# Kernel optimization log

Measured on AMD Instinct MI355X. Metric: run time of the kernel, lower is better.

## Reference

```python
import jax, jax.numpy as jnp
import numpy as np

N = 10000      # nodes
E = 160000     # edges (before self loops)
F_IN = 78      # atom features
C = 128        # output_dim per head
H = 10         # heads in gat1
G = 64         # graphs in batch


def gat_conv(x, src, dst, n_nodes, W, a_src, a_dst, heads, ch):
    # x: [N, Fin]; W: [Fin, heads*ch]; a_src/a_dst: [heads, ch]
    h = (x @ W).reshape(-1, heads, ch)                      # [N, H, C]
    alpha_src = (h * a_src).sum(-1)                         # [N, H]
    alpha_dst = (h * a_dst).sum(-1)                         # [N, H]
    e = jax.nn.leaky_relu(alpha_src[src] + alpha_dst[dst], 0.2)  # [E, H]
    # segment softmax over edges grouped by destination node
    m = jax.ops.segment_max(e, dst, num_segments=n_nodes)
    m = jnp.where(jnp.isfinite(m), m, 0.0)
    ex = jnp.exp(e - m[dst])
    den = jax.ops.segment_sum(ex, dst, num_segments=n_nodes)
    alpha = ex / (den[dst] + 1e-16)                         # [E, H]
    out = jax.ops.segment_sum(h[src] * alpha[:, :, None], dst,
                              num_segments=n_nodes)          # [N, H, C]
    return out, alpha


def setup_inputs() -> dict:
    key = jax.random.key(0)
    ks = jax.random.split(key, 12)
    x = jax.random.normal(ks[0], (N, F_IN), dtype=jnp.float32)
    edge_index = jax.random.randint(ks[1], (2, E), 0, N, dtype=jnp.int64)
    batch = jnp.sort(jax.random.randint(ks[2], (N,), 0, G, dtype=jnp.int64))
    s1 = 1.0 / np.sqrt(F_IN)
    s2 = 1.0 / np.sqrt(H * C)
    W1 = jax.random.normal(ks[3], (F_IN, H * C), jnp.float32) * s1
    att_src1 = jax.random.normal(ks[4], (H, C), jnp.float32) * 0.1
    att_dst1 = jax.random.normal(ks[5], (H, C), jnp.float32) * 0.1
    b1 = jnp.zeros((H * C,), jnp.float32)
    W2 = jax.random.normal(ks[6], (H * C, C), jnp.float32) * s2
    att_src2 = jax.random.normal(ks[7], (1, C), jnp.float32) * 0.1
    att_dst2 = jax.random.normal(ks[8], (1, C), jnp.float32) * 0.1
    b2 = jnp.zeros((C,), jnp.float32)
    return {"x": x, "edge_index": edge_index, "batch": batch,
            "W1": W1, "att_src1": att_src1, "att_dst1": att_dst1, "b1": b1,
            "W2": W2, "att_src2": att_src2, "att_dst2": att_dst2, "b2": b2}


def reference(x, edge_index, batch, W1, att_src1, att_dst1, b1,
              W2, att_src2, att_dst2, b2):
    n = x.shape[0]
    loops = jnp.arange(n, dtype=edge_index.dtype)
    src = jnp.concatenate([edge_index[0], loops])  # PyG adds self loops
    dst = jnp.concatenate([edge_index[1], loops])
    # layer 1: 10 heads, concat
    h1, alpha1 = gat_conv(x, src, dst, n, W1, att_src1, att_dst1, H, C)
    h1 = jax.nn.elu(h1.reshape(n, H * C) + b1)     # dropout skipped (eval)
    # layer 2: 1 head
    h2, _ = gat_conv(h1, src, dst, n, W2, att_src2, att_dst2, 1, C)
    h2 = jax.nn.elu(h2.reshape(n, C) + b2)
    # global max pool per graph
    pooled = jax.ops.segment_max(h2, batch, num_segments=G)  # [G, C]
    return pooled, alpha1
```

## Files before the change

kernel.cpp:

```cpp
#include <hip/hip_runtime.h>
#include <hip/hip_bf16.h>

#define FIN 78
#define CDIM 128
#define HEADS 10
#define HC 1280
#define GRAPHS 64
#define KP 96

typedef __bf16 bf16x8 __attribute__((ext_vector_type(8)));
typedef __bf16 bf16x4 __attribute__((ext_vector_type(4)));
typedef float f32x4 __attribute__((ext_vector_type(4)));

__global__ void init_kernel(unsigned* counts, unsigned* cursor, unsigned* pooled_u,
                            float* as1, float* ad1,
                            const float* __restrict__ x, __bf16* __restrict__ xb,
                            const float* __restrict__ W1, __bf16* __restrict__ W1t,
                            const float* __restrict__ W2, __bf16* __restrict__ W2t,
                            int N, int Mpad) {
    int t = blockIdx.x * 256 + threadIdx.x;
    if (t < N) { counts[t] = 0u; cursor[t] = 0u; }
    if (t < GRAPHS * CDIM) pooled_u[t] = 0x007FFFFFu;
    if (t < N * HEADS) { as1[t] = 0.f; ad1[t] = 0.f; }
    if (t < Mpad * KP) {
        int m = t / KP, k = t % KP;
        float v = (m < N && k < FIN) ? x[(size_t)m * FIN + k] : 0.f;
        xb[t] = (__bf16)v;
    }
    if (t < HC * KP) {
        int n = t / KP, k = t % KP;
        float v = (k < FIN) ? W1[(size_t)k * HC + n] : 0.f;
        W1t[t] = (__bf16)v;
    }
    if (t < CDIM * HC) {
        int n = t / HC, k = t % HC;
        W2t[t] = (__bf16)W2[(size_t)k * CDIM + n];
    }
}

__global__ __launch_bounds__(256) void gemm1_mfma_kernel(
        const __bf16* __restrict__ xb, const __bf16* __restrict__ W1t,
        const float* __restrict__ asrc, const float* __restrict__ adst,
        __bf16* __restrict__ h1pb, float* __restrict__ as1, float* __restrict__ ad1,
        int M) {
    __shared__ __align__(16) __bf16 smem[2 * 128 * 104];
    auto Alds = (__bf16 (*)[104])smem;
    auto Blds = (__bf16 (*)[104])(smem + 128 * 104);
    const int tid = threadIdx.x;
    const int wave = tid >> 6, lane = tid & 63;
    const int wr = wave >> 1, wc = wave & 1;
    const int m0 = blockIdx.x * 128;
    const int head = blockIdx.y;
    const int n0 = head * CDIM;
    const int fl = lane & 15;
    const int fh = lane >> 4;

    for (int idx = tid; idx < 128 * 12; idx += 256) {
        int r = idx / 12, ks = (idx % 12) * 8;
        *(bf16x8*)&Alds[r][ks] = *(const bf16x8*)(xb + (size_t)(m0 + r) * KP + ks);
        *(bf16x8*)&Blds[r][ks] = *(const bf16x8*)(W1t + (size_t)(n0 + r) * KP + ks);
    }
    __syncthreads();

    f32x4 acc[4][4] = {};
    #pragma unroll
    for (int ks = 0; ks < KP; ks += 32) {
        bf16x8 a[4], b[4];
        #pragma unroll
        for (int t = 0; t < 4; ++t) {
            a[t] = *(const bf16x8*)&Alds[wr * 64 + t * 16 + fl][ks + fh * 8];
            b[t] = *(const bf16x8*)&Blds[wc * 64 + t * 16 + fl][ks + fh * 8];
        }
        #pragma unroll
        for (int i = 0; i < 4; ++i)
            #pragma unroll
            for (int j = 0; j < 4; ++j)
                acc[i][j] = __builtin_amdgcn_mfma_f32_16x16x32_bf16(a[i], b[j], acc[i][j], 0, 0, 0);
    }

    float a_s[4], a_d[4];
    #pragma unroll
    for (int j = 0; j < 4; ++j) {
        int gn = n0 + wc * 64 + j * 16 + fl;
        a_s[j] = asrc[gn];
        a_d[j] = adst[gn];
    }
    #pragma unroll
    for (int i = 0; i < 4; ++i) {
        #pragma unroll
        for (int r = 0; r < 4; ++r) {
            int gm = m0 + wr * 64 + i * 16 + fh * 4 + r;
            float vs = 0.f, vd = 0.f;
            #pragma unroll
            for (int j = 0; j < 4; ++j) {
                vs += acc[i][j][r] * a_s[j];
                vd += acc[i][j][r] * a_d[j];
            }
            #pragma unroll
            for (int off = 1; off < 16; off <<= 1) {
                vs += __shfl_xor(vs, off);
                vd += __shfl_xor(vd, off);
            }
            if (fl == 0 && gm < M) {
                atomicAdd(&as1[gm * HEADS + head], vs);
                atomicAdd(&ad1[gm * HEADS + head], vd);
            }
        }
    }

    __syncthreads();
    auto Cst = (__bf16 (*)[136])smem;
    #pragma unroll
    for (int i = 0; i < 4; ++i)
        #pragma unroll
        for (int j = 0; j < 4; ++j)
            #pragma unroll
            for (int r = 0; r < 4; ++r)
                Cst[wr * 64 + i * 16 + fh * 4 + r][wc * 64 + j * 16 + fl] = (__bf16)acc[i][j][r];
    __syncthreads();
    for (int idx = tid; idx < 128 * 16; idx += 256) {
        int r = idx >> 4, v = (idx & 15) * 8;
        int gm = m0 + r;
        if (gm < M)
            *(bf16x8*)(h1pb + (size_t)gm * HC + n0 + v) = *(const bf16x8*)&Cst[r][v];
    }
}

__global__ __launch_bounds__(256) void gemm2_mfma_kernel(
        const __bf16* __restrict__ A, const __bf16* __restrict__ W2t,
        float* __restrict__ Cpart, int M) {
    constexpr int BK = 64;
    constexpr int KCHUNK = HC / 2;
    __shared__ __align__(16) __bf16 smem[2 * 64 * 72];
    auto Alds = (__bf16 (*)[72])smem;
    auto Blds = (__bf16 (*)[72])(smem + 64 * 72);
    const int tid = threadIdx.x;
    const int wave = tid >> 6, lane = tid & 63;
    const int wr = wave >> 1, wc = wave & 1;
    const int m0 = blockIdx.x * 64;
    const int n0 = blockIdx.y * 64;
    const int kbase = blockIdx.z * KCHUNK;

    const int kslot = (tid & 7) * 8;
    const int srow  = tid >> 3;
    const int fl = lane & 15;
    const int fh = lane >> 4;

    f32x4 acc[2][2] = {};

    for (int k0 = kbase; k0 < kbase + KCHUNK; k0 += BK) {
        #pragma unroll
        for (int rp = 0; rp < 2; ++rp) {
            int r = srow + rp * 32;
            int gm = m0 + r;
            bf16x8 va = {};
            if (gm < M) va = *(const bf16x8*)(A + (size_t)gm * HC + k0 + kslot);
            *(bf16x8*)&Alds[r][kslot] = va;
            *(bf16x8*)&Blds[r][kslot] = *(const bf16x8*)(W2t + (size_t)(n0 + r) * HC + k0 + kslot);
        }
        __syncthreads();
        #pragma unroll
        for (int ks = 0; ks < BK; ks += 32) {
            bf16x8 a[2], b[2];
            #pragma unroll
            for (int t = 0; t < 2; ++t) {
                a[t] = *(const bf16x8*)&Alds[wr * 32 + t * 16 + fl][ks + fh * 8];
                b[t] = *(const bf16x8*)&Blds[wc * 32 + t * 16 + fl][ks + fh * 8];
            }
            #pragma unroll
            for (int i = 0; i < 2; ++i)
                #pragma unroll
                for (int j = 0; j < 2; ++j)
                    acc[i][j] = __builtin_amdgcn_mfma_f32_16x16x32_bf16(a[i], b[j], acc[i][j], 0, 0, 0);
        }
        __syncthreads();
    }
    auto CstF = (float (*)[68])smem;
    #pragma unroll
    for (int i = 0; i < 2; ++i)
        #pragma unroll
        for (int j = 0; j < 2; ++j)
            #pragma unroll
            for (int r = 0; r < 4; ++r)
                CstF[wr * 32 + i * 16 + fh * 4 + r][wc * 32 + j * 16 + fl] = acc[i][j][r];
    __syncthreads();
    float* base = Cpart + (size_t)blockIdx.z * M * CDIM;
    for (int idx = tid; idx < 64 * 16; idx += 256) {
        int r = idx >> 4, c = (idx & 15) * 4;
        int gm = m0 + r;
        if (gm < M)
            *(f32x4*)(base + (size_t)gm * CDIM + n0 + c) = *(const f32x4*)&CstF[r][c];
    }
}

__global__ __launch_bounds__(256) void combine_kernel(
        const float* __restrict__ Cpart, const float* __restrict__ asrc2,
        const float* __restrict__ adst2, __bf16* __restrict__ h2b,
        float* __restrict__ as2, float* __restrict__ ad2, int N) {
    const int lane = threadIdx.x & 63, wave = threadIdx.x >> 6;
    const int n = blockIdx.x * 4 + wave;
    if (n >= N) return;
    const float* p0 = Cpart + (size_t)n * CDIM;
    const float* p1 = Cpart + (size_t)(N + n) * CDIM;
    float v0 = p0[lane] + p1[lane];
    float v1 = p0[lane + 64] + p1[lane + 64];
    h2b[(size_t)n * CDIM + lane] = (__bf16)v0;
    h2b[(size_t)n * CDIM + lane + 64] = (__bf16)v1;
    float vs = v0 * asrc2[lane] + v1 * asrc2[lane + 64];
    float vd = v0 * adst2[lane] + v1 * adst2[lane + 64];
    #pragma unroll
    for (int off = 32; off; off >>= 1) {
        vs += __shfl_xor(vs, off);
        vd += __shfl_xor(vd, off);
    }
    if (lane == 0) { as2[n] = vs; ad2[n] = vd; }
}

__global__ void hist_kernel(const int* __restrict__ ei, int E, int N, unsigned* counts) {
    int e = blockIdx.x * 256 + threadIdx.x;
    int Et = E + N;
    if (e >= Et) return;
    int d = (e < E) ? ei[E + e] : (e - E);
    atomicAdd(&counts[d], 1u);
}

__global__ void scan_kernel(const unsigned* __restrict__ counts, unsigned* __restrict__ offsets, int n) {
    __shared__ unsigned part[1024];
    int t = threadIdx.x;
    int chunk = (n + 1023) / 1024;
    int lo = t * chunk, hi = min(lo + chunk, n);
    unsigned s = 0;
    for (int i = lo; i < hi; ++i) s += counts[i];
    part[t] = s;
    __syncthreads();
    for (int d = 1; d < 1024; d <<= 1) {
        unsigned v = (t >= d) ? part[t - d] : 0u;
        __syncthreads();
        part[t] += v;
        __syncthreads();
    }
    unsigned base = (t == 0) ? 0u : part[t - 1];
    for (int i = lo; i < hi; ++i) { offsets[i] = base; base += counts[i]; }
    if (t == 1023) offsets[n] = part[1023];
}

__global__ void scatter_kernel(const int* __restrict__ ei, int E, int N,
                               const unsigned* __restrict__ offsets, unsigned* cursor,
                               int2* __restrict__ csr2) {
    int e = blockIdx.x * 256 + threadIdx.x;
    int Et = E + N;
    if (e >= Et) return;
    int s, d;
    if (e < E) { s = ei[e]; d = ei[E + e]; } else { s = e - E; d = e - E; }
    unsigned pos = offsets[d] + atomicAdd(&cursor[d], 1u);
    csr2[pos] = make_int2(s, e);
}

__global__ __launch_bounds__(256) void softmax1_kernel(
        const unsigned* __restrict__ offsets, const int2* __restrict__ csr2,
        const float* __restrict__ as1, const float* __restrict__ ad1,
        float* __restrict__ alpha_out, float* __restrict__ alpha_csr, int N) {
    const int wave = threadIdx.x >> 6, lane = threadIdx.x & 63;
    const int n = blockIdx.x * 4 + wave;
    if (n >= N) return;
    const unsigned p0 = offsets[n], p1 = offsets[n + 1];
    const unsigned deg = p1 - p0;

    float adn[HEADS];
    #pragma unroll
    for (int h = 0; h < HEADS; ++h) adn[h] = ad1[n * HEADS + h];

    if (deg <= 64) {
        const bool act = lane < (int)deg;
        const unsigned p = p0 + lane;
        int s = 0, eid = 0;
        if (act) { int2 se = csr2[p]; s = se.x; eid = se.y; }
        const float* arow = as1 + (size_t)s * HEADS;
        float e[HEADS];
        #pragma unroll
        for (int h = 0; h < HEADS; ++h) {
            float v = act ? (arow[h] + adn[h]) : -INFINITY;
            e[h] = (v >= 0.f) ? v : 0.2f * v;
        }
        float m[HEADS];
        #pragma unroll
        for (int h = 0; h < HEADS; ++h) m[h] = e[h];
        #pragma unroll
        for (int off = 32; off; off >>= 1)
            #pragma unroll
            for (int h = 0; h < HEADS; ++h) m[h] = fmaxf(m[h], __shfl_xor(m[h], off));
        float ex[HEADS], sm[HEADS];
        #pragma unroll
        for (int h = 0; h < HEADS; ++h) {
            ex[h] = act ? __expf(e[h] - m[h]) : 0.f;
            sm[h] = ex[h];
        }
        #pragma unroll
        for (int off = 32; off; off >>= 1)
            #pragma unroll
            for (int h = 0; h < HEADS; ++h) sm[h] += __shfl_xor(sm[h], off);
        if (act) {
            #pragma unroll
            for (int h = 0; h < HEADS; ++h) {
                float a = ex[h] / (sm[h] + 1e-16f);
                alpha_csr[(size_t)p * HEADS + h] = a;
                alpha_out[(size_t)eid * HEADS + h] = a;
            }
        }
    } else {
        float m[HEADS];
        #pragma unroll
        for (int h = 0; h < HEADS; ++h) m[h] = -INFINITY;
        for (unsigned p = p0 + lane; p < p1; p += 64) {
            const float* arow = as1 + (size_t)csr2[p].x * HEADS;
            #pragma unroll
            for (int h = 0; h < HEADS; ++h) {
                float v = arow[h] + adn[h];
                v = (v >= 0.f) ? v : 0.2f * v;
                m[h] = fmaxf(m[h], v);
            }
        }
        #pragma unroll
        for (int off = 32; off; off >>= 1)
            #pragma unroll
            for (int h = 0; h < HEADS; ++h) m[h] = fmaxf(m[h], __shfl_xor(m[h], off));
        float sm[HEADS];
        #pragma unroll
        for (int h = 0; h < HEADS; ++h) sm[h] = 0.f;
        for (unsigned p = p0 + lane; p < p1; p += 64) {
            const float* arow = as1 + (size_t)csr2[p].x * HEADS;
            #pragma unroll
            for (int h = 0; h < HEADS; ++h) {
                float v = arow[h] + adn[h];
                v = (v >= 0.f) ? v : 0.2f * v;
                sm[h] += __expf(v - m[h]);
            }
        }
        #pragma unroll
        for (int off = 32; off; off >>= 1)
            #pragma unroll
            for (int h = 0; h < HEADS; ++h) sm[h] += __shfl_xor(sm[h], off);
        float inv[HEADS];
        #pragma unroll
        for (int h = 0; h < HEADS; ++h) inv[h] = 1.f / (sm[h] + 1e-16f);
        for (unsigned p = p0 + lane; p < p1; p += 64) {
            int2 se = csr2[p];
            const float* arow = as1 + (size_t)se.x * HEADS;
            #pragma unroll
            for (int h = 0; h < HEADS; ++h) {
                float v = arow[h] + adn[h];
                v = (v >= 0.f) ? v : 0.2f * v;
                float a = __expf(v - m[h]) * inv[h];
                alpha_csr[(size_t)p * HEADS + h] = a;
                alpha_out[(size_t)se.y * HEADS + h] = a;
            }
        }
    }
}

__global__ __launch_bounds__(160) void agg1_kernel(
        const unsigned* __restrict__ offsets, const int2* __restrict__ csr2,
        const float* __restrict__ alpha_csr, const __bf16* __restrict__ h1pb,
        const float* __restrict__ b1, __bf16* __restrict__ h1b, int N) {
    __shared__ float a_lds[64 * HEADS];
    __shared__ int s_lds[64];
    int n = blockIdx.x;
    unsigned p0 = offsets[n], p1 = offsets[n + 1];
    int tid = threadIdx.x;
    const int col = tid * 8;
    const int hd = tid >> 4;
    float acc[8] = {};
    for (unsigned base = p0; base < p1; base += 64) {
        int cnt = (int)min(64u, p1 - base);
        for (int idx = tid; idx < cnt * HEADS; idx += 160)
            a_lds[idx] = alpha_csr[(size_t)base * HEADS + idx];
        for (int idx = tid; idx < cnt; idx += 160) s_lds[idx] = csr2[base + idx].x;
        __syncthreads();
        #pragma unroll 2
        for (int j = 0; j < cnt; ++j) {
            bf16x8 hv = *(const bf16x8*)(h1pb + (size_t)s_lds[j] * HC + col);
            float a = a_lds[j * HEADS + hd];
            #pragma unroll
            for (int k = 0; k < 8; ++k) acc[k] += (float)hv[k] * a;
        }
        __syncthreads();
    }
    const float4 bv0 = *(const float4*)(b1 + col);
    const float4 bv1 = *(const float4*)(b1 + col + 4);
    float vb[8] = {bv0.x, bv0.y, bv0.z, bv0.w, bv1.x, bv1.y, bv1.z, bv1.w};
    bf16x8 outv;
    #pragma unroll
    for (int k = 0; k < 8; ++k) {
        float v = acc[k] + vb[k];
        v = (v > 0.f) ? v : expm1f(v);
        outv[k] = (__bf16)v;
    }
    *(bf16x8*)(h1b + (size_t)n * HC + col) = outv;
}

__device__ __forceinline__ unsigned enc_f(float f) {
    unsigned b = __float_as_uint(f);
    return (b & 0x80000000u) ? ~b : (b | 0x80000000u);
}
__device__ __forceinline__ float dec_f(unsigned k) {
    return (k & 0x80000000u) ? __uint_as_float(k & 0x7FFFFFFFu) : __uint_as_float(~k);
}

__global__ __launch_bounds__(128) void agg2_kernel(
        const unsigned* __restrict__ offsets, const int2* __restrict__ csr2,
        const float* __restrict__ as2, const float* __restrict__ ad2,
        const __bf16* __restrict__ h2b, const float* __restrict__ b2,
        const int* __restrict__ batch, unsigned* __restrict__ pooled_u, int N) {
    const int n = blockIdx.x;
    const int tid = threadIdx.x;
    const int lane = tid & 63;
    const unsigned p0 = offsets[n], p1 = offsets[n + 1];
    const int deg = (int)(p1 - p0);
    const float adn = ad2[n];
    float acc = 0.f;

    if (deg <= 64) {
        int s_reg = 0;
        float e_reg = -INFINITY;
        if (lane < deg) {
            s_reg = csr2[p0 + lane].x;
            float v = as2[s_reg] + adn;
            e_reg = (v >= 0.f) ? v : 0.2f * v;
        }
        float m = e_reg;
        #pragma unroll
        for (int off = 32; off; off >>= 1) m = fmaxf(m, __shfl_xor(m, off));
        float ex = (lane < deg) ? __expf(e_reg - m) : 0.f;
        float den = ex;
        #pragma unroll
        for (int off = 32; off; off >>= 1) den += __shfl_xor(den, off);
        float inv = 1.f / (den + 1e-16f);
        for (int j = 0; j < deg; ++j) {
            int sj = __shfl(s_reg, j);
            float aj = __shfl(ex, j) * inv;
            acc += (float)h2b[(size_t)sj * CDIM + tid] * aj;
        }
    } else {
        float m = -INFINITY;
        for (unsigned p = p0 + lane; p < p1; p += 64) {
            float v = as2[csr2[p].x] + adn;
            v = (v >= 0.f) ? v : 0.2f * v;
            m = fmaxf(m, v);
        }
        #pragma unroll
        for (int off = 32; off; off >>= 1) m = fmaxf(m, __shfl_xor(m, off));
        float den = 0.f;
        for (unsigned p = p0 + lane; p < p1; p += 64) {
            float v = as2[csr2[p].x] + adn;
            v = (v >= 0.f) ? v : 0.2f * v;
            den += __expf(v - m);
        }
        #pragma unroll
        for (int off = 32; off; off >>= 1) den += __shfl_xor(den, off);
        float inv = 1.f / (den + 1e-16f);
        for (unsigned p = p0; p < p1; ++p) {
            int sj = csr2[p].x;
            float v = as2[sj] + adn;
            v = (v >= 0.f) ? v : 0.2f * v;
            float aj = __expf(v - m) * inv;
            acc += (float)h2b[(size_t)sj * CDIM + tid] * aj;
        }
    }
    float v = acc + b2[tid];
    v = (v > 0.f) ? v : expm1f(v);
    atomicMax(&pooled_u[batch[n] * CDIM + tid], enc_f(v));
}

__global__ void pool_write_kernel(const unsigned* __restrict__ pooled_u, float* __restrict__ out) {
    int t = blockIdx.x * 256 + threadIdx.x;
    if (t < GRAPHS * CDIM) out[t] = dec_f(pooled_u[t]);
}

extern "C" void kernel_launch(void* const* d_in, const int* in_sizes, int n_in,
                              void* d_out, int out_size, void* d_ws, size_t ws_size,
                              hipStream_t stream) {
    const float* x     = (const float*)d_in[0];
    const int*   ei    = (const int*)d_in[1];
    const int*   batch = (const int*)d_in[2];
    const float* W1    = (const float*)d_in[3];
    const float* asrc1 = (const float*)d_in[4];
    const float* adst1 = (const float*)d_in[5];
    const float* b1    = (const float*)d_in[6];
    const float* W2    = (const float*)d_in[7];
    const float* asrc2 = (const float*)d_in[8];
    const float* adst2 = (const float*)d_in[9];
    const float* b2    = (const float*)d_in[10];
    float* out = (float*)d_out;

    const int N  = in_sizes[0] / FIN;
    const int E  = in_sizes[1] / 2;
    const int Et = E + N;
    const int Mpad = ((N + 127) / 128) * 128;

    char* w = (char*)d_ws;
    auto alloc = [&](size_t nbytes) {
        char* p = w;
        w += (nbytes + 255) & ~(size_t)255;
        return p;
    };
    __bf16* h1pb = (__bf16*)alloc((size_t)N * HC * 2);
    __bf16* h1b  = (__bf16*)alloc((size_t)N * HC * 2);
    __bf16* xb   = (__bf16*)alloc((size_t)Mpad * KP * 2);
    __bf16* W1t  = (__bf16*)alloc((size_t)HC * KP * 2);
    __bf16* W2t  = (__bf16*)alloc((size_t)CDIM * HC * 2);
    float*  Cpart = (float*)alloc((size_t)2 * N * CDIM * 4);
    __bf16* h2b  = (__bf16*)alloc((size_t)N * CDIM * 2);
    float*  as1  = (float*)alloc((size_t)N * HEADS * 4);
    float*  ad1  = (float*)alloc((size_t)N * HEADS * 4);
    float*  as2  = (float*)alloc((size_t)N * 4);
    float*  ad2  = (float*)alloc((size_t)N * 4);
    float*  alpha_csr = (float*)alloc((size_t)Et * HEADS * 4);
    unsigned* counts  = (unsigned*)alloc((size_t)N * 4);
    unsigned* cursor  = (unsigned*)alloc((size_t)N * 4);
    unsigned* offsets = (unsigned*)alloc((size_t)(N + 1) * 4);
    int2* csr2 = (int2*)alloc((size_t)Et * 8);
    unsigned* pooled_u = (unsigned*)alloc((size_t)GRAPHS * CDIM * 4);

    float* alpha_out = out + GRAPHS * CDIM;

    const int init_work = Mpad * KP;
    init_kernel<<<(init_work + 255) / 256, 256, 0, stream>>>(
        counts, cursor, pooled_u, as1, ad1, x, xb, W1, W1t, W2, W2t, N, Mpad);

    gemm1_mfma_kernel<<<dim3(Mpad / 128, HEADS), 256, 0, stream>>>(
        xb, W1t, asrc1, adst1, h1pb, as1, ad1, N);

    hist_kernel<<<(Et + 255) / 256, 256, 0, stream>>>(ei, E, N, counts);
    scan_kernel<<<1, 1024, 0, stream>>>(counts, offsets, N);
    scatter_kernel<<<(Et + 255) / 256, 256, 0, stream>>>(ei, E, N, offsets, cursor, csr2);

    softmax1_kernel<<<(N + 3) / 4, 256, 0, stream>>>(
        offsets, csr2, as1, ad1, alpha_out, alpha_csr, N);
    agg1_kernel<<<N, 160, 0, stream>>>(offsets, csr2, alpha_csr, h1pb, b1, h1b, N);

    gemm2_mfma_kernel<<<dim3((N + 63) / 64, CDIM / 64, 2), 256, 0, stream>>>(
        h1b, W2t, Cpart, N);
    combine_kernel<<<(N + 3) / 4, 256, 0, stream>>>(Cpart, asrc2, adst2, h2b, as2, ad2, N);

    agg2_kernel<<<N, 128, 0, stream>>>(offsets, csr2, as2, ad2, h2b, b2, batch, pooled_u, N);

    pool_write_kernel<<<(GRAPHS * CDIM + 255) / 256, 256, 0, stream>>>(pooled_u, out);
}
```

Measured before the change: 271.2 us.

## Split agg1 across eight column blocks per node and fold self-loops into scan

The layer-1 aggregation now launches eight blocks per node, each covering 160 columns with one scalar bf16 column per thread, in place of one block doing 8-wide vector loads. This raises parallelism and occupancy, but it loses vectorized loads and makes each block re-read the CSR source indices and reload alpha values. Self-loop counting moves out of the histogram kernel and into the scan as a +1 per node, which shortens the atomic histogram pass.

```diff
diff --git a/kernel.cpp b/kernel.cpp
--- a/kernel.cpp
+++ b/kernel.cpp
@@ -36,6 +36,11 @@
         int n = t / HC, k = t % HC;
         W2t[t] = (__bf16)W2[(size_t)k * CDIM + n];
     }
+}
+
+__global__ void hist_kernel(const int* __restrict__ ei, int E, unsigned* counts) {
+    int e = blockIdx.x * 256 + threadIdx.x;
+    if (e < E) atomicAdd(&counts[ei[E + e]], 1u);
 }
 
 __global__ __launch_bounds__(256) void gemm1_mfma_kernel(
@@ -216,21 +221,13 @@
     if (lane == 0) { as2[n] = vs; ad2[n] = vd; }
 }
 
-__global__ void hist_kernel(const int* __restrict__ ei, int E, int N, unsigned* counts) {
-    int e = blockIdx.x * 256 + threadIdx.x;
-    int Et = E + N;
-    if (e >= Et) return;
-    int d = (e < E) ? ei[E + e] : (e - E);
-    atomicAdd(&counts[d], 1u);
-}
-
 __global__ void scan_kernel(const unsigned* __restrict__ counts, unsigned* __restrict__ offsets, int n) {
     __shared__ unsigned part[1024];
     int t = threadIdx.x;
     int chunk = (n + 1023) / 1024;
     int lo = t * chunk, hi = min(lo + chunk, n);
     unsigned s = 0;
-    for (int i = lo; i < hi; ++i) s += counts[i];
+    for (int i = lo; i < hi; ++i) s += counts[i] + 1u;
     part[t] = s;
     __syncthreads();
     for (int d = 1; d < 1024; d <<= 1) {
@@ -240,7 +237,7 @@
         __syncthreads();
     }
     unsigned base = (t == 0) ? 0u : part[t - 1];
-    for (int i = lo; i < hi; ++i) { offsets[i] = base; base += counts[i]; }
+    for (int i = lo; i < hi; ++i) { offsets[i] = base; base += counts[i] + 1u; }
     if (t == 1023) offsets[n] = part[1023];
 }
 
@@ -362,40 +359,34 @@
         const unsigned* __restrict__ offsets, const int2* __restrict__ csr2,
         const float* __restrict__ alpha_csr, const __bf16* __restrict__ h1pb,
         const float* __restrict__ b1, __bf16* __restrict__ h1b, int N) {
-    __shared__ float a_lds[64 * HEADS];
+    __shared__ float a_lds[64 * 2];
     __shared__ int s_lds[64];
-    int n = blockIdx.x;
-    unsigned p0 = offsets[n], p1 = offsets[n + 1];
-    int tid = threadIdx.x;
-    const int col = tid * 8;
-    const int hd = tid >> 4;
-    float acc[8] = {};
+    const int c = blockIdx.x & 7;
+    const int n = blockIdx.x >> 3;
+    const int tid = threadIdx.x;
+    const int col = c * 160 + tid;
+    const int h0 = (c * 160) >> 7;
+    const int hl = (col >> 7) - h0;
+    const unsigned p0 = offsets[n], p1 = offsets[n + 1];
+    float acc = 0.f;
     for (unsigned base = p0; base < p1; base += 64) {
         int cnt = (int)min(64u, p1 - base);
-        for (int idx = tid; idx < cnt * HEADS; idx += 160)
-            a_lds[idx] = alpha_csr[(size_t)base * HEADS + idx];
+        for (int idx = tid; idx < cnt * 2; idx += 160) {
+            int j = idx >> 1, hh = idx & 1;
+            a_lds[idx] = alpha_csr[(size_t)(base + j) * HEADS + h0 + hh];
+        }
         for (int idx = tid; idx < cnt; idx += 160) s_lds[idx] = csr2[base + idx].x;
         __syncthreads();
-        #pragma unroll 2
+        #pragma unroll 4
         for (int j = 0; j < cnt; ++j) {
-            bf16x8 hv = *(const bf16x8*)(h1pb + (size_t)s_lds[j] * HC + col);
-            float a = a_lds[j * HEADS + hd];
-            #pragma unroll
-            for (int k = 0; k < 8; ++k) acc[k] += (float)hv[k] * a;
+            float hv = (float)h1pb[(size_t)s_lds[j] * HC + col];
+            acc += hv * a_lds[j * 2 + hl];
         }
         __syncthreads();
     }
-    const float4 bv0 = *(const float4*)(b1 + col);
-    const float4 bv1 = *(const float4*)(b1 + col + 4);
-    float vb[8] = {bv0.x, bv0.y, bv0.z, bv0.w, bv1.x, bv1.y, bv1.z, bv1.w};
-    bf16x8 outv;
-    #pragma unroll
-    for (int k = 0; k < 8; ++k) {
-        float v = acc[k] + vb[k];
-        v = (v > 0.f) ? v : expm1f(v);
-        outv[k] = (__bf16)v;
-    }
-    *(bf16x8*)(h1b + (size_t)n * HC + col) = outv;
+    float v = acc + b1[col];
+    v = (v > 0.f) ? v : expm1f(v);
+    h1b[(size_t)n * HC + col] = (__bf16)v;
 }
 
 __device__ __forceinline__ unsigned enc_f(float f) {
@@ -530,13 +521,13 @@
     gemm1_mfma_kernel<<<dim3(Mpad / 128, HEADS), 256, 0, stream>>>(
         xb, W1t, asrc1, adst1, h1pb, as1, ad1, N);
 
-    hist_kernel<<<(Et + 255) / 256, 256, 0, stream>>>(ei, E, N, counts);
+    hist_kernel<<<(E + 255) / 256, 256, 0, stream>>>(ei, E, counts);
     scan_kernel<<<1, 1024, 0, stream>>>(counts, offsets, N);
     scatter_kernel<<<(Et + 255) / 256, 256, 0, stream>>>(ei, E, N, offsets, cursor, csr2);
 
     softmax1_kernel<<<(N + 3) / 4, 256, 0, stream>>>(
         offsets, csr2, as1, ad1, alpha_out, alpha_csr, N);
-    agg1_kernel<<<N, 160, 0, stream>>>(offsets, csr2, alpha_csr, h1pb, b1, h1b, N);
+    agg1_kernel<<<N * 8, 160, 0, stream>>>(offsets, csr2, alpha_csr, h1pb, b1, h1b, N);
 
     gemm2_mfma_kernel<<<dim3((N + 63) / 64, CDIM / 64, 2), 256, 0, stream>>>(
         h1b, W2t, Cpart, N);
```

New measurement: 323.0 us. 1.19x slower.
